# Optimization experiments

Measured on AMD Instinct MI355X. Metric: run time of the kernel, lower is better.

The kernel has to match this reference:

```python
import jax, jax.numpy as jnp
import numpy as np

NUM_HEADS = 16
THETA = 1000.0


def apply_rope(x, positions, theta):
    """x: [B, H, S, d_k]; positions: [S] float. Interleaved-pair RoPE."""
    d = x.shape[-1]
    inv_freq = theta ** (-jnp.arange(0, d, 2, dtype=x.dtype) / d)  # [d/2]
    ang = positions[:, None] * inv_freq[None, :]                    # [S, d/2]
    cos, sin = jnp.cos(ang), jnp.sin(ang)
    x1, x2 = x[..., 0::2], x[..., 1::2]
    r1 = x1 * cos - x2 * sin
    r2 = x1 * sin + x2 * cos
    return jnp.stack([r1, r2], axis=-1).reshape(x.shape)


def setup_inputs() -> dict:
    key = jax.random.key(0)
    ks = jax.random.split(key, 5)
    B, S, D = 2, 2048, 1024
    scale = 1.0 / np.sqrt(D)
    return {
        "in_features": jax.random.normal(ks[0], (B, S, D), jnp.float32),
        "q_proj_weight": jax.random.normal(ks[1], (D, D), jnp.float32) * scale,
        "k_proj_weight": jax.random.normal(ks[2], (D, D), jnp.float32) * scale,
        "v_proj_weight": jax.random.normal(ks[3], (D, D), jnp.float32) * scale,
        "o_proj_weight": jax.random.normal(ks[4], (D, D), jnp.float32) * scale,
        "token_positions": jnp.arange(S, dtype=jnp.int32),
    }


def reference(in_features, q_proj_weight, k_proj_weight, v_proj_weight,
              o_proj_weight, token_positions):
    B, S, D = in_features.shape
    H = NUM_HEADS
    d_k = D // H

    # Original rearrange: '(d_k heads) d_model -> heads d_model d_k'
    # => first dim splits as [d_k, heads] (heads is the inner factor).
    def split_heads(w):
        return w.reshape(d_k, H, D).transpose(1, 2, 0)  # [H, D, d_k]

    Wq, Wk, Wv = split_heads(q_proj_weight), split_heads(k_proj_weight), split_heads(v_proj_weight)

    xq = jnp.einsum("bsd,hdk->bhsk", in_features, Wq)
    xk = jnp.einsum("bsd,hdk->bhsk", in_features, Wk)
    xv = jnp.einsum("bsd,hdk->bhsk", in_features, Wv)

    pos = token_positions.astype(in_features.dtype)
    xq = apply_rope(xq, pos, THETA)
    xk = apply_rope(xk, pos, THETA)

    scores = jnp.einsum("bhqk,bhmk->bhqm", xq, xk) / jnp.sqrt(
        jnp.asarray(d_k, in_features.dtype))
    causal_mask = jnp.triu(jnp.ones((S, S), bool), k=1)  # True above diagonal
    scores = jnp.where(causal_mask, -jnp.inf, scores)
    attn = jax.nn.softmax(scores, axis=-1)

    out = jnp.einsum("bhqm,bhmv->bhqv", attn, xv)        # [B, H, S, d_k]
    out = out.transpose(0, 2, 1, 3).reshape(B, S, D)     # (heads d_emb) concat
    return out @ o_proj_weight                            # [B, S, d_o]
```

## Files before the change

### kernel.cpp

```cpp
#include <hip/hip_runtime.h>

typedef unsigned short u16;
typedef unsigned int u32;
typedef __bf16 bf16x8 __attribute__((ext_vector_type(8)));
typedef float f32x4 __attribute__((ext_vector_type(4)));

#define SEQ 2048
#define DMODEL 1024
#define NH 16
#define DK 64
#define BATCH 2
#define MTOT (BATCH * SEQ)

__device__ __forceinline__ u16 f2b(float f) {
  u32 u = __float_as_uint(f);
  u += 0x7fffu + ((u >> 16) & 1u);
  return (u16)(u >> 16);
}

__device__ __forceinline__ u32 cvtpk(float lo, float hi) {
  u32 r;
  asm("v_cvt_pk_bf16_f32 %0, %1, %2" : "=v"(r) : "v"(lo), "v"(hi));
  return r;
}

__device__ __forceinline__ void gload16(const void* g, void* l) {
  __builtin_amdgcn_global_load_lds((const __attribute__((address_space(1))) u32*)g,
                                   (__attribute__((address_space(3))) u32*)l, 16, 0, 0);
}

__global__ __launch_bounds__(256) void cvt_all(
    const float* __restrict__ X, const float* __restrict__ wq,
    const float* __restrict__ wk, const float* __restrict__ wv,
    const int* __restrict__ tokpos, u16* __restrict__ Xb,
    u16* __restrict__ oq, u16* __restrict__ ok, u16* __restrict__ ov,
    float2* __restrict__ tab) {
  const int bid = blockIdx.x;
  if (bid < 7168) {
    const float* in;
    u16* out;
    int i;
    if (bid < 4096) {
      in = X; out = Xb; i = bid * 256 + threadIdx.x;
    } else {
      const int j = bid - 4096;
      const int m = j >> 10;
      in = (m == 0) ? wq : ((m == 1) ? wk : wv);
      out = (m == 0) ? oq : ((m == 1) ? ok : ov);
      i = (j & 1023) * 256 + threadIdx.x;
    }
    float4 v = ((const float4*)in)[i];
    uint2 o;
    o.x = (u32)f2b(v.x) | ((u32)f2b(v.y) << 16);
    o.y = (u32)f2b(v.z) | ((u32)f2b(v.w) << 16);
    ((uint2*)out)[i] = o;
  } else {
    const int i = (bid - 7168) * 256 + threadIdx.x;
    const int s = i >> 5, Xi = i & 31;
    const float invf = powf(1000.0f, -(float)Xi / 32.0f);
    const float ang = (float)tokpos[s] * invf;
    float sn, cs;
    sincosf(ang, &sn, &cs);
    tab[i] = make_float2(cs, sn);
  }
}

__global__ __launch_bounds__(256) void transpose_wo(const float* __restrict__ wo,
                                                    u16* __restrict__ wot) {
  __shared__ float tile[32][33];
  const int bx = blockIdx.x * 32;
  const int by = blockIdx.y * 32;
  const int tx = threadIdx.x & 31, ty = threadIdx.x >> 5;
  for (int j = ty; j < 32; j += 8)
    tile[j][tx] = wo[(size_t)(by + j) * DMODEL + bx + tx];
  __syncthreads();
  for (int j = ty; j < 32; j += 8)
    wot[(size_t)(bx + j) * DMODEL + by + tx] = f2b(tile[tx][j]);
}

__device__ __forceinline__ void qkv_core(const u16* __restrict__ A,
                                         const u16* __restrict__ Bt,
                                         int mbase, int nbase,
                                         u16* As, u16* Bs, f32x4 acc[4][4]) {
  const int t = threadIdx.x;
  const int lane = t & 63, w = t >> 6;
  const int wr = w >> 1, wc = w & 1;
  const int l15 = lane & 15, lg = lane >> 4;
  const int srow = t >> 3;
  const int sch = (t & 7) ^ (srow & 7);
  const int rsw = l15 & 7;
  const int ASZ = 128 * 64;
  const int NIT = DMODEL / 64;

  auto stage = [&](int bufsel, int kb) {
    u16* Ad = &As[bufsel * ASZ];
    u16* Bd = &Bs[bufsel * ASZ];
#pragma unroll
    for (int j = 0; j < 4; ++j)
      gload16(&A[(size_t)(mbase + srow + 32 * j) * DMODEL + kb + sch * 8],
              &Ad[j * 2048 + t * 8]);
#pragma unroll
    for (int j = 0; j < 4; ++j)
      gload16(&Bt[(size_t)(nbase + srow + 32 * j) * DMODEL + kb + sch * 8],
              &Bd[j * 2048 + t * 8]);
  };

  auto compute = [&](int bufsel) {
    const u16* Ac = &As[bufsel * ASZ];
    const u16* Bc = &Bs[bufsel * ASZ];
#pragma unroll
    for (int kk = 0; kk < 2; ++kk) {
      bf16x8 af[4], bfr[4];
#pragma unroll
      for (int mi = 0; mi < 4; ++mi) {
        const int row = wr * 64 + mi * 16 + l15;
        af[mi] = *(const bf16x8*)&Ac[row * 64 + (((kk * 4 + lg) ^ rsw) * 8)];
      }
#pragma unroll
      for (int ni = 0; ni < 4; ++ni) {
        const int row = wc * 64 + ni * 16 + l15;
        bfr[ni] = *(const bf16x8*)&Bc[row * 64 + (((kk * 4 + lg) ^ rsw) * 8)];
      }
#pragma unroll
      for (int mi = 0; mi < 4; ++mi)
#pragma unroll
        for (int ni = 0; ni < 4; ++ni)
          acc[mi][ni] =
              __builtin_amdgcn_mfma_f32_16x16x32_bf16(af[mi], bfr[ni], acc[mi][ni], 0, 0, 0);
    }
  };

  stage(0, 0);

  for (int it = 0; it < NIT - 1; ++it) {
    const int buf = it & 1;
    stage(buf ^ 1, (it + 1) * 64);
    __builtin_amdgcn_sched_barrier(0);
    asm volatile("s_waitcnt vmcnt(8)" ::: "memory");
    __builtin_amdgcn_sched_barrier(0);
    __builtin_amdgcn_s_barrier();
    __builtin_amdgcn_sched_barrier(0);
    compute(buf);
    __builtin_amdgcn_sched_barrier(0);
    __builtin_amdgcn_s_barrier();
  }
  asm volatile("s_waitcnt vmcnt(0)" ::: "memory");
  __builtin_amdgcn_sched_barrier(0);
  __builtin_amdgcn_s_barrier();
  __builtin_amdgcn_sched_barrier(0);
  compute((DMODEL / 64 - 1) & 1);
}

__global__ __launch_bounds__(256) void gemm_qkv(
    const u16* __restrict__ Xb, const u16* __restrict__ Wqb,
    const u16* __restrict__ Wkb, const u16* __restrict__ Wvb,
    u16* __restrict__ Qb, u16* __restrict__ Kb, u16* __restrict__ Vb,
    const float2* __restrict__ tab) {
  __shared__ __align__(16) u16 As[2 * 128 * 64];
  __shared__ __align__(16) u16 Bs[2 * 128 * 64];

  const int mat = blockIdx.y >> 3;
  const int nbase = (blockIdx.y & 7) * 128;
  const int mbase = blockIdx.x * 128;
  const u16* Bt = (mat == 0) ? Wqb : ((mat == 1) ? Wkb : Wvb);

  f32x4 acc[4][4];
#pragma unroll
  for (int mi = 0; mi < 4; ++mi)
#pragma unroll
    for (int ni = 0; ni < 4; ++ni) {
      f32x4 z = {0.f, 0.f, 0.f, 0.f};
      acc[mi][ni] = z;
    }

  qkv_core(Xb, Bt, mbase, nbase, As, Bs, acc);

  const int t = threadIdx.x;
  const int lane = t & 63, w = t >> 6;
  const int wr = w >> 1, wc = w & 1;
  const int l15 = lane & 15, lg = lane >> 4;

  if (mat == 2) {
#pragma unroll
    for (int mi = 0; mi < 4; ++mi) {
#pragma unroll
      for (int r = 0; r < 4; ++r) {
        const int row = mbase + wr * 64 + mi * 16 + lg * 4 + r;
        const int bi = row >> 11, s = row & (SEQ - 1);
#pragma unroll
        for (int ni = 0; ni < 4; ++ni) {
          const int c = nbase + wc * 64 + ni * 16 + l15;
          const int hh = c & 15, vd = c >> 4;
          Vb[((size_t)((bi * NH + hh) * DK + vd)) * SEQ + s] = f2b(acc[mi][ni][r]);
        }
      }
    }
  } else {
    u16* Ob = (mat == 0) ? Qb : Kb;
    const float qscale = (mat == 0) ? 0.125f * 1.44269504088896f : 1.0f;
#pragma unroll
    for (int ni = 0; ni < 4; ni += 2) {
      const int Xi = (nbase + wc * 64 + ni * 16) >> 5;
#pragma unroll
      for (int mi = 0; mi < 4; ++mi) {
#pragma unroll
        for (int r = 0; r < 4; ++r) {
          const int row = mbase + wr * 64 + mi * 16 + lg * 4 + r;
          const int bi = row >> 11, s = row & (SEQ - 1);
          const float2 ct = tab[(s << 5) + Xi];
          const float x1 = acc[mi][ni][r], x2 = acc[mi][ni + 1][r];
          const float r1 = (x1 * ct.x - x2 * ct.y) * qscale;
          const float r2 = (x1 * ct.y + x2 * ct.x) * qscale;
          const u32 pk = (u32)f2b(r1) | ((u32)f2b(r2) << 16);
          *(u32*)&Ob[((size_t)((bi * NH + l15) * SEQ + s) << 6) + (Xi << 1)] = pk;
        }
      }
    }
  }
}

__global__ __launch_bounds__(256, 5) void flash_attn(
    const u16* __restrict__ Qg, const u16* __restrict__ Kg,
    const u16* __restrict__ VTg, u16* __restrict__ Ag) {
  __shared__ __align__(16) u16 Ks[64 * 64];
  __shared__ __align__(16) u16 Vs[80 * 64];
  __shared__ __align__(16) u16 Ps[4][16][72];

  const int id = blockIdx.y * 32 + blockIdx.x;
  const int within = id >> 3;
  const int bh = (id & 7) * 4 + (within & 3);
  const int qt = 31 - (within >> 2);
  const int b = bh >> 4, h = bh & 15;
  const int qbase = qt * 64;

  const size_t hoff = (size_t)bh * SEQ * DK;
  const u16* Qh = Qg + hoff;
  const u16* Kh = Kg + hoff;
  const u16* VTh = VTg + hoff;

  const int t = threadIdx.x;
  const int lane = t & 63, w = t >> 6;
  const int l15 = lane & 15, lg = lane >> 4;
  const int sw = l15 & 7;

  for (int i = t; i < 16 * 64; i += 256) {
    const int rr = i >> 6, cc = i & 63;
    Vs[(64 + rr) * 64 + cc] = (rr == 0) ? (u16)0x3F80 : (u16)0;
  }

  const int qrow = qbase + w * 16 + l15;
  const bf16x8 qf0 = *(const bf16x8*)&Qh[(size_t)qrow * DK + lg * 8];
  const bf16x8 qf1 = *(const bf16x8*)&Qh[(size_t)qrow * DK + 32 + lg * 8];

  f32x4 oaccT[4];
  f32x4 oacc5;
#pragma unroll
  for (int vf = 0; vf < 4; ++vf) {
    f32x4 z = {0.f, 0.f, 0.f, 0.f};
    oaccT[vf] = z;
  }
  {
    f32x4 z = {0.f, 0.f, 0.f, 0.f};
    oacc5 = z;
  }

  const int srow = t >> 3;
  const int sc = ((t & 7) ^ (srow & 7)) * 8;

  for (int kt = 0; kt <= qt; ++kt) {
    const int kvbase = kt * 64;
    __syncthreads();
    gload16(&Kh[(size_t)(kvbase + srow) * DK + sc], &Ks[t * 8]);
    gload16(&Kh[(size_t)(kvbase + srow + 32) * DK + sc], &Ks[2048 + t * 8]);
    gload16(&VTh[(size_t)srow * SEQ + kvbase + sc], &Vs[t * 8]);
    gload16(&VTh[(size_t)(srow + 32) * SEQ + kvbase + sc], &Vs[2048 + t * 8]);
    asm volatile("s_waitcnt vmcnt(0)" ::: "memory");
    __builtin_amdgcn_s_barrier();

    f32x4 sT[4];
    __builtin_amdgcn_s_setprio(1);
#pragma unroll
    for (int f = 0; f < 4; ++f) {
      const int row = f * 16 + l15;
      bf16x8 k0 = *(const bf16x8*)&Ks[row * 64 + (lg ^ sw) * 8];
      bf16x8 k1 = *(const bf16x8*)&Ks[row * 64 + ((4 + lg) ^ sw) * 8];
      f32x4 z = {0.f, 0.f, 0.f, 0.f};
      z = __builtin_amdgcn_mfma_f32_16x16x32_bf16(k0, qf0, z, 0, 0, 0);
      z = __builtin_amdgcn_mfma_f32_16x16x32_bf16(k1, qf1, z, 0, 0, 0);
      sT[f] = z;
    }
    __builtin_amdgcn_s_setprio(0);

    if (kt == qt) {
#pragma unroll
      for (int f = 0; f < 4; ++f)
#pragma unroll
        for (int r = 0; r < 4; ++r) {
          const int kvc = kvbase + f * 16 + lg * 4 + r;
          if (kvc > qrow) sT[f][r] = -1e30f;
        }
    }

#pragma unroll
    for (int f = 0; f < 4; ++f)
#pragma unroll
      for (int r = 0; r < 4; ++r) sT[f][r] = exp2f(sT[f][r]);

#pragma unroll
    for (int f = 0; f < 4; ++f) {
      uint2 pkv;
      pkv.x = cvtpk(sT[f][0], sT[f][1]);
      pkv.y = cvtpk(sT[f][2], sT[f][3]);
      *(uint2*)&Ps[w][l15][f * 16 + lg * 4] = pkv;
    }

    __builtin_amdgcn_s_setprio(1);
#pragma unroll
    for (int c = 0; c < 2; ++c) {
      const bf16x8 pb = *(const bf16x8*)&Ps[w][l15][c * 32 + lg * 8];
#pragma unroll
      for (int vf = 0; vf < 4; ++vf) {
        const bf16x8 va =
            *(const bf16x8*)&Vs[(vf * 16 + l15) * 64 + ((c * 4 + lg) ^ sw) * 8];
        oaccT[vf] = __builtin_amdgcn_mfma_f32_16x16x32_bf16(va, pb, oaccT[vf], 0, 0, 0);
      }
      const bf16x8 va5 =
          *(const bf16x8*)&Vs[(64 + l15) * 64 + ((c * 4 + lg) ^ sw) * 8];
      oacc5 = __builtin_amdgcn_mfma_f32_16x16x32_bf16(va5, pb, oacc5, 0, 0, 0);
    }
    __builtin_amdgcn_s_setprio(0);
  }

  const float l = __shfl(oacc5[0], l15);
  const float inv = 1.0f / l;
  const size_t base = ((size_t)(b * SEQ + qrow)) * DMODEL + h * DK;
#pragma unroll
  for (int vf = 0; vf < 4; ++vf) {
    uint2 ov;
    ov.x = cvtpk(oaccT[vf][0] * inv, oaccT[vf][1] * inv);
    ov.y = cvtpk(oaccT[vf][2] * inv, oaccT[vf][3] * inv);
    *(uint2*)&Ag[base + vf * 16 + lg * 4] = ov;
  }
}

__global__ __launch_bounds__(256) void gemm_out(const u16* __restrict__ Ab,
                                                const u16* __restrict__ Wotb,
                                                float* __restrict__ Co) {
  __shared__ __align__(16) u16 As[64 * 64];
  __shared__ __align__(16) u16 Bs[128 * 64];
  const int mbase = blockIdx.x * 64, nbase = blockIdx.y * 128;

  const int t = threadIdx.x;
  const int lane = t & 63, w = t >> 6;
  const int wr = w >> 1, wc = w & 1;
  const int l15 = lane & 15, lg = lane >> 4;
  const int srow = t >> 3;
  const int sch = (t & 7) ^ (srow & 7);
  const int rsw = l15 & 7;

  f32x4 acc[2][4];
#pragma unroll
  for (int mi = 0; mi < 2; ++mi)
#pragma unroll
    for (int ni = 0; ni < 4; ++ni) {
      f32x4 z = {0.f, 0.f, 0.f, 0.f};
      acc[mi][ni] = z;
    }

  for (int kb = 0; kb < DMODEL; kb += 64) {
    gload16(&Ab[(size_t)(mbase + srow) * DMODEL + kb + sch * 8], &As[t * 8]);
    gload16(&Ab[(size_t)(mbase + 32 + srow) * DMODEL + kb + sch * 8], &As[2048 + t * 8]);
#pragma unroll
    for (int j = 0; j < 4; ++j)
      gload16(&Wotb[(size_t)(nbase + srow + 32 * j) * DMODEL + kb + sch * 8],
              &Bs[j * 2048 + t * 8]);
    __syncthreads();
#pragma unroll
    for (int kk = 0; kk < 2; ++kk) {
      bf16x8 af[2], bfr[4];
#pragma unroll
      for (int mi = 0; mi < 2; ++mi) {
        const int row = wr * 32 + mi * 16 + l15;
        af[mi] = *(const bf16x8*)&As[row * 64 + (((kk * 4 + lg) ^ rsw) * 8)];
      }
#pragma unroll
      for (int ni = 0; ni < 4; ++ni) {
        const int row = wc * 64 + ni * 16 + l15;
        bfr[ni] = *(const bf16x8*)&Bs[row * 64 + (((kk * 4 + lg) ^ rsw) * 8)];
      }
#pragma unroll
      for (int mi = 0; mi < 2; ++mi)
#pragma unroll
        for (int ni = 0; ni < 4; ++ni)
          acc[mi][ni] =
              __builtin_amdgcn_mfma_f32_16x16x32_bf16(af[mi], bfr[ni], acc[mi][ni], 0, 0, 0);
    }
    __syncthreads();
  }

#pragma unroll
  for (int mi = 0; mi < 2; ++mi) {
#pragma unroll
    for (int r = 0; r < 4; ++r) {
      const int row = mbase + wr * 32 + mi * 16 + lg * 4 + r;
#pragma unroll
      for (int ni = 0; ni < 4; ++ni) {
        const int c = nbase + wc * 64 + ni * 16 + l15;
        Co[(size_t)row * DMODEL + c] = acc[mi][ni][r];
      }
    }
  }
}

extern "C" void kernel_launch(void* const* d_in, const int* in_sizes, int n_in,
                              void* d_out, int out_size, void* d_ws, size_t ws_size,
                              hipStream_t stream) {
  const float* X = (const float*)d_in[0];
  const float* Wq = (const float*)d_in[1];
  const float* Wk = (const float*)d_in[2];
  const float* Wv = (const float*)d_in[3];
  const float* Wo = (const float*)d_in[4];
  const int* tokpos = (const int*)d_in[5];
  float* out = (float*)d_out;

  u16* p = (u16*)d_ws;
  u16* Xb = p;   p += (size_t)MTOT * DMODEL;
  u16* Wqb = p;  p += (size_t)DMODEL * DMODEL;
  u16* Wkb = p;  p += (size_t)DMODEL * DMODEL;
  u16* Wvb = p;  p += (size_t)DMODEL * DMODEL;
  u16* Wotb = p; p += (size_t)DMODEL * DMODEL;
  u16* Qb = p;   p += (size_t)BATCH * NH * SEQ * DK;
  u16* Kb = p;   p += (size_t)BATCH * NH * SEQ * DK;
  u16* Vb = p;   p += (size_t)BATCH * NH * SEQ * DK;
  float2* tab = (float2*)(p + 512);
  u16* Ab = Xb;

  cvt_all<<<7424, 256, 0, stream>>>(X, Wq, Wk, Wv, tokpos, Xb, Wqb, Wkb, Wvb, tab);
  transpose_wo<<<dim3(32, 32), 256, 0, stream>>>(Wo, Wotb);

  gemm_qkv<<<dim3(32, 24), 256, 0, stream>>>(Xb, Wqb, Wkb, Wvb, Qb, Kb, Vb, tab);
  flash_attn<<<dim3(32, 32), 256, 0, stream>>>(Qb, Kb, Vb, Ab);
  gemm_out<<<dim3(64, 8), 256, 0, stream>>>(Ab, Wotb, out);
}
```

Baseline: 127.4 us.

## Shrink QKV GEMM tile to 64x128 and drop double-buffered pipeline

The QKV projection GEMM moves from 128x128 double-buffered tiles to 64x128 single-buffered tiles with plain __syncthreads, doubling the grid to 64x24 blocks and raising launch bounds to 6 blocks per CU. The aim is more blocks across the 256 CUs (the old grid of 768 blocks fills them unevenly) and higher occupancy from fewer registers and less LDS. In exchange, global-load latency is no longer overlapped with MFMA within a block, and each block has lower arithmetic intensity, so weight tiles are reloaded more often.

```diff
diff --git a/kernel.cpp b/kernel.cpp
--- a/kernel.cpp
+++ b/kernel.cpp
@@ -78,10 +78,19 @@
     wot[(size_t)(bx + j) * DMODEL + by + tx] = f2b(tile[tx][j]);
 }
 
-__device__ __forceinline__ void qkv_core(const u16* __restrict__ A,
-                                         const u16* __restrict__ Bt,
-                                         int mbase, int nbase,
-                                         u16* As, u16* Bs, f32x4 acc[4][4]) {
+__global__ __launch_bounds__(256, 6) void gemm_qkv(
+    const u16* __restrict__ Xb, const u16* __restrict__ Wqb,
+    const u16* __restrict__ Wkb, const u16* __restrict__ Wvb,
+    u16* __restrict__ Qb, u16* __restrict__ Kb, u16* __restrict__ Vb,
+    const float2* __restrict__ tab) {
+  __shared__ __align__(16) u16 As[64 * 64];
+  __shared__ __align__(16) u16 Bs[128 * 64];
+
+  const int mat = blockIdx.y >> 3;
+  const int nbase = (blockIdx.y & 7) * 128;
+  const int mbase = blockIdx.x * 64;
+  const u16* Bt = (mat == 0) ? Wqb : ((mat == 1) ? Wkb : Wvb);
+
   const int t = threadIdx.x;
   const int lane = t & 63, w = t >> 6;
   const int wr = w >> 1, wc = w & 1;
@@ -89,103 +98,53 @@
   const int srow = t >> 3;
   const int sch = (t & 7) ^ (srow & 7);
   const int rsw = l15 & 7;
-  const int ASZ = 128 * 64;
-  const int NIT = DMODEL / 64;
-
-  auto stage = [&](int bufsel, int kb) {
-    u16* Ad = &As[bufsel * ASZ];
-    u16* Bd = &Bs[bufsel * ASZ];
-#pragma unroll
-    for (int j = 0; j < 4; ++j)
-      gload16(&A[(size_t)(mbase + srow + 32 * j) * DMODEL + kb + sch * 8],
-              &Ad[j * 2048 + t * 8]);
+
+  f32x4 acc[2][4];
+#pragma unroll
+  for (int mi = 0; mi < 2; ++mi)
+#pragma unroll
+    for (int ni = 0; ni < 4; ++ni) {
+      f32x4 z = {0.f, 0.f, 0.f, 0.f};
+      acc[mi][ni] = z;
+    }
+
+  for (int kb = 0; kb < DMODEL; kb += 64) {
+    gload16(&Xb[(size_t)(mbase + srow) * DMODEL + kb + sch * 8], &As[t * 8]);
+    gload16(&Xb[(size_t)(mbase + 32 + srow) * DMODEL + kb + sch * 8], &As[2048 + t * 8]);
 #pragma unroll
     for (int j = 0; j < 4; ++j)
       gload16(&Bt[(size_t)(nbase + srow + 32 * j) * DMODEL + kb + sch * 8],
-              &Bd[j * 2048 + t * 8]);
-  };
-
-  auto compute = [&](int bufsel) {
-    const u16* Ac = &As[bufsel * ASZ];
-    const u16* Bc = &Bs[bufsel * ASZ];
+              &Bs[j * 2048 + t * 8]);
+    __syncthreads();
 #pragma unroll
     for (int kk = 0; kk < 2; ++kk) {
-      bf16x8 af[4], bfr[4];
-#pragma unroll
-      for (int mi = 0; mi < 4; ++mi) {
-        const int row = wr * 64 + mi * 16 + l15;
-        af[mi] = *(const bf16x8*)&Ac[row * 64 + (((kk * 4 + lg) ^ rsw) * 8)];
+      bf16x8 af[2], bfr[4];
+#pragma unroll
+      for (int mi = 0; mi < 2; ++mi) {
+        const int row = wr * 32 + mi * 16 + l15;
+        af[mi] = *(const bf16x8*)&As[row * 64 + (((kk * 4 + lg) ^ rsw) * 8)];
       }
 #pragma unroll
       for (int ni = 0; ni < 4; ++ni) {
         const int row = wc * 64 + ni * 16 + l15;
-        bfr[ni] = *(const bf16x8*)&Bc[row * 64 + (((kk * 4 + lg) ^ rsw) * 8)];
-      }
-#pragma unroll
-      for (int mi = 0; mi < 4; ++mi)
+        bfr[ni] = *(const bf16x8*)&Bs[row * 64 + (((kk * 4 + lg) ^ rsw) * 8)];
+      }
+#pragma unroll
+      for (int mi = 0; mi < 2; ++mi)
 #pragma unroll
         for (int ni = 0; ni < 4; ++ni)
           acc[mi][ni] =
               __builtin_amdgcn_mfma_f32_16x16x32_bf16(af[mi], bfr[ni], acc[mi][ni], 0, 0, 0);
     }
-  };
-
-  stage(0, 0);
-
-  for (int it = 0; it < NIT - 1; ++it) {
-    const int buf = it & 1;
-    stage(buf ^ 1, (it + 1) * 64);
-    __builtin_amdgcn_sched_barrier(0);
-    asm volatile("s_waitcnt vmcnt(8)" ::: "memory");
-    __builtin_amdgcn_sched_barrier(0);
-    __builtin_amdgcn_s_barrier();
-    __builtin_amdgcn_sched_barrier(0);
-    compute(buf);
-    __builtin_amdgcn_sched_barrier(0);
-    __builtin_amdgcn_s_barrier();
-  }
-  asm volatile("s_waitcnt vmcnt(0)" ::: "memory");
-  __builtin_amdgcn_sched_barrier(0);
-  __builtin_amdgcn_s_barrier();
-  __builtin_amdgcn_sched_barrier(0);
-  compute((DMODEL / 64 - 1) & 1);
-}
-
-__global__ __launch_bounds__(256) void gemm_qkv(
-    const u16* __restrict__ Xb, const u16* __restrict__ Wqb,
-    const u16* __restrict__ Wkb, const u16* __restrict__ Wvb,
-    u16* __restrict__ Qb, u16* __restrict__ Kb, u16* __restrict__ Vb,
-    const float2* __restrict__ tab) {
-  __shared__ __align__(16) u16 As[2 * 128 * 64];
-  __shared__ __align__(16) u16 Bs[2 * 128 * 64];
-
-  const int mat = blockIdx.y >> 3;
-  const int nbase = (blockIdx.y & 7) * 128;
-  const int mbase = blockIdx.x * 128;
-  const u16* Bt = (mat == 0) ? Wqb : ((mat == 1) ? Wkb : Wvb);
-
-  f32x4 acc[4][4];
-#pragma unroll
-  for (int mi = 0; mi < 4; ++mi)
-#pragma unroll
-    for (int ni = 0; ni < 4; ++ni) {
-      f32x4 z = {0.f, 0.f, 0.f, 0.f};
-      acc[mi][ni] = z;
-    }
-
-  qkv_core(Xb, Bt, mbase, nbase, As, Bs, acc);
-
-  const int t = threadIdx.x;
-  const int lane = t & 63, w = t >> 6;
-  const int wr = w >> 1, wc = w & 1;
-  const int l15 = lane & 15, lg = lane >> 4;
+    __syncthreads();
+  }
 
   if (mat == 2) {
 #pragma unroll
-    for (int mi = 0; mi < 4; ++mi) {
+    for (int mi = 0; mi < 2; ++mi) {
 #pragma unroll
       for (int r = 0; r < 4; ++r) {
-        const int row = mbase + wr * 64 + mi * 16 + lg * 4 + r;
+        const int row = mbase + wr * 32 + mi * 16 + lg * 4 + r;
         const int bi = row >> 11, s = row & (SEQ - 1);
 #pragma unroll
         for (int ni = 0; ni < 4; ++ni) {
@@ -202,10 +161,10 @@
     for (int ni = 0; ni < 4; ni += 2) {
       const int Xi = (nbase + wc * 64 + ni * 16) >> 5;
 #pragma unroll
-      for (int mi = 0; mi < 4; ++mi) {
+      for (int mi = 0; mi < 2; ++mi) {
 #pragma unroll
         for (int r = 0; r < 4; ++r) {
-          const int row = mbase + wr * 64 + mi * 16 + lg * 4 + r;
+          const int row = mbase + wr * 32 + mi * 16 + lg * 4 + r;
           const int bi = row >> 11, s = row & (SEQ - 1);
           const float2 ct = tab[(s << 5) + Xi];
           const float x1 = acc[mi][ni][r], x2 = acc[mi][ni + 1][r];
@@ -438,7 +397,7 @@
   cvt_all<<<7424, 256, 0, stream>>>(X, Wq, Wk, Wv, tokpos, Xb, Wqb, Wkb, Wvb, tab);
   transpose_wo<<<dim3(32, 32), 256, 0, stream>>>(Wo, Wotb);
 
-  gemm_qkv<<<dim3(32, 24), 256, 0, stream>>>(Xb, Wqb, Wkb, Wvb, Qb, Kb, Vb, tab);
+  gemm_qkv<<<dim3(64, 24), 256, 0, stream>>>(Xb, Wqb, Wkb, Wvb, Qb, Kb, Vb, tab);
   flash_attn<<<dim3(32, 32), 256, 0, stream>>>(Qb, Kb, Vb, Ab);
   gemm_out<<<dim3(64, 8), 256, 0, stream>>>(Ab, Wotb, out);
 }
```

Result: faster. 118.8 us (-6.8%).
